# Kernel optimization log

Measured on AMD Instinct MI355X. Metric: run time of the kernel, lower is better.

## Reference

```python
import jax, jax.numpy as jnp
import numpy as np

B, T, DM, DS = 8, 2048, 1024, 256
BASE_DECAY = 0.05


def _lin(k, out_dim, in_dim):
    return jax.random.normal(k, (out_dim, in_dim), jnp.float32) / np.sqrt(in_dim).astype(np.float32)


def setup_inputs() -> dict:
    key = jax.random.key(0)
    ks = jax.random.split(key, 18)
    return {
        "x": jax.random.normal(ks[0], (B, T, DM), jnp.float32),
        "prev_state": jax.random.normal(ks[1], (B, DS), jnp.float32),
        "W_in": _lin(ks[2], DS, DM),
        "W_x": _lin(ks[3], DS, DM),
        "W_s": _lin(ks[4], DS, DS),
        "W_out": _lin(ks[5], DM, DS),
        "W_gx": _lin(ks[6], DS, DM),
        "b_gx": jax.random.normal(ks[7], (DS,), jnp.float32) * 0.02,
        "W_gs": _lin(ks[8], DS, DS),
        "b_gs": jax.random.normal(ks[9], (DS,), jnp.float32) * 0.02,
        "W_dc": _lin(ks[10], DS, DM + DS),
        "b_dc": jax.random.normal(ks[11], (DS,), jnp.float32) * 0.02,
        "W_pp": _lin(ks[12], DS, 2 * DS),
        "b_pp": jax.random.normal(ks[13], (DS,), jnp.float32) * 0.02,
        "W_pg": _lin(ks[14], DS, DS),
        "b_pg": jax.random.normal(ks[15], (DS,), jnp.float32) * 0.02,
    }


def reference(x, prev_state, W_in, W_x, W_s, W_out, W_gx, b_gx, W_gs, b_gs,
              W_dc, b_dc, W_pp, b_pp, W_pg, b_pg):
    # torch Linear: y = x @ W.T (+ b); W is [out, in]
    lin = lambda v, W: jnp.einsum('bti,oi->bto', v, W)
    Bx, Tx, _ = x.shape
    delta = lin(x, W_in)                                   # [B,T,DS]
    s_prev = jnp.broadcast_to(prev_state[:, None, :], (Bx, Tx, prev_state.shape[-1]))
    ctx = jnp.concatenate([x, s_prev], axis=-1)            # [B,T,DM+DS]
    decay = jnp.exp(-BASE_DECAY * jnp.clip(jax.nn.sigmoid(lin(ctx, W_dc) + b_dc), 0.0, 1.0))
    s_pred = s_prev * decay + delta + lin(x, W_x) + 0.5 * lin(s_prev, W_s)
    perturb_in = jnp.concatenate([s_pred, s_prev], axis=-1)  # [B,T,2*DS]
    perturb_vec = jnp.tanh(lin(perturb_in, W_pp) + b_pp)
    perturb_strength = jax.nn.sigmoid(lin(s_prev, W_pg) + b_pg)
    s_corrected = s_pred + perturb_strength * perturb_vec
    gate_in = jax.nn.sigmoid(lin(x, W_gx) + b_gx)
    gate_state = jax.nn.sigmoid(lin(s_prev, W_gs) + b_gs)
    h = s_corrected * gate_in * gate_state
    out = lin(h, W_out)                                    # [B,T,DM]
    return out, h[:, -1, :]
```

## Files before the change

kernel.cpp:

```cpp
#include <hip/hip_runtime.h>
#include <hip/hip_bf16.h>
#include <math.h>


typedef __attribute__((ext_vector_type(4)))  float f32x4;
typedef __attribute__((ext_vector_type(8)))  short bf16x8;

#define DEV static __device__ __forceinline__

DEV float bf2f(short u) {
  union { float f; unsigned i; } v; v.i = ((unsigned)(unsigned short)u) << 16; return v.f;
}
DEV short f2bf(float f) {
  union { float f; unsigned i; } v; v.f = f;
  unsigned x = v.i;
  return (short)((x + 0x7fffu + ((x >> 16) & 1u)) >> 16);
}
DEV unsigned pk_bf16(float lo, float hi) {
  __hip_bfloat162 h = __float22bfloat162_rn(make_float2(lo, hi));
  return *(unsigned*)&h;
}
DEV float sigmoidf_(float x) { return 1.f / (1.f + expf(-x)); }

DEV void gl16(const void* g, void* l) {
  __builtin_amdgcn_global_load_lds(
      (const __attribute__((address_space(1))) void*)(g),
      (__attribute__((address_space(3))) void*)(l), 16, 0, 0);
}

static const size_t OFF_S    = 0;
static const size_t OFF_G    = 8388608;
static const size_t OFF_H    = 16777216;
static const size_t OFF_WCAT = 25165824;
static const size_t OFF_WPP  = OFF_WCAT + 1572864;
static const size_t OFF_WOUT = OFF_WPP + 131072;
static const size_t OFF_VEC  = OFF_WOUT + 524288;

__global__ __launch_bounds__(256, 1) void prep_ws_k(
    const float* __restrict__ W_in, const float* __restrict__ W_x,
    const float* __restrict__ W_gx, const float* __restrict__ W_dc,
    const float* __restrict__ W_pp, const float* __restrict__ W_out,
    short* __restrict__ wcat, short* __restrict__ wpp, short* __restrict__ wout,
    const float* __restrict__ prev, const float* __restrict__ Ws,
    const float* __restrict__ bdc, const float* __restrict__ bpp,
    const float* __restrict__ Wpg, const float* __restrict__ bpg,
    const float* __restrict__ Wgs, const float* __restrict__ bgs,
    float* __restrict__ vecs) {
  const int bid = (int)blockIdx.x, tid = (int)threadIdx.x;
  if (bid < 4352) {
    const int idx = bid * 256 + tid;
    const int N_WCAT = 768 * 1024, N_WPP = 256 * 256;
    if (idx < N_WCAT) {
      const int r = idx >> 10, k = idx & 1023;
      const int g = r / 192, j = r % 192;
      float v;
      if (j < 64)       v = W_in[(g * 64 + j) * 1024 + k] + W_x[(g * 64 + j) * 1024 + k];
      else if (j < 128) v = W_gx[(g * 64 + j - 64) * 1024 + k];
      else              v = W_dc[(g * 64 + j - 128) * 1280 + k];
      wcat[idx] = f2bf(v);
    } else if (idx < N_WCAT + N_WPP) {
      const int j = idx - N_WCAT, o = j >> 8, k = j & 255;
      wpp[j] = f2bf(W_pp[o * 512 + k]);
    } else {
      const int j = idx - N_WCAT - N_WPP, o = j >> 8, k = j & 255;
      wout[j] = f2bf(W_out[o * 256 + k]);
    }
  } else {
    const int sb = bid - 4352;
    const int b = sb / 20, rem = sb % 20, m = rem >> 2, oq = rem & 3;
    const int lane = tid & 63, w = tid >> 6;
    const float4 sv = *(const float4*)(prev + b * 256 + lane * 4);
    const float* Wb; const float* bias; int stride, off;
    if (m == 0)      { Wb = W_dc; stride = 1280; off = 1024; bias = bdc; }
    else if (m == 1) { Wb = Ws;   stride = 256;  off = 0;    bias = nullptr; }
    else if (m == 2) { Wb = W_pp; stride = 512;  off = 256;  bias = bpp; }
    else if (m == 3) { Wb = Wpg;  stride = 256;  off = 0;    bias = bpg; }
    else             { Wb = Wgs;  stride = 256;  off = 0;    bias = bgs; }
    const int o0 = oq * 64 + w * 16;
#pragma unroll 4
    for (int i = 0; i < 16; ++i) {
      const int o = o0 + i;
      const float4 wv = *(const float4*)(Wb + (size_t)o * stride + off + lane * 4);
      float p = wv.x * sv.x + wv.y * sv.y + wv.z * sv.z + wv.w * sv.w;
#pragma unroll
      for (int d = 32; d >= 1; d >>= 1) p += __shfl_xor(p, d, 64);
      if (lane == 0) {
        float r = (m == 1) ? 0.5f * p : p + bias[o];
        if (m >= 3) r = sigmoidf_(r);
        vecs[m * 2048 + b * 256 + o] = r;
      }
    }
  }
}

__global__ __launch_bounds__(512) void gemm1sg_k(const float* __restrict__ X,
                                                 const short* __restrict__ Bm,
                                                 const float* __restrict__ prev,
                                                 const float* __restrict__ bgx,
                                                 const float* __restrict__ vecs,
                                                 short* __restrict__ S,
                                                 short* __restrict__ G) {
  __shared__ short As[2][8192];
  __shared__ short Bs[2][12288];
  const int tid = (int)threadIdx.x, lane = tid & 63, w = tid >> 6;
  int bid = (int)blockIdx.x;
  bid = (bid & 7) * 64 + (bid >> 3);
  const int mt = bid >> 2, grp = bid & 3;
  const int m0 = mt * 128, b = m0 >> 11;
  const short* gB = Bm + (size_t)(grp * 192) * 1024;

  const int GrA[2] = {tid, 512 + tid};
  const int rA0 = GrA[0] >> 3, gA0 = (GrA[0] & 7) ^ (rA0 & 7);
  const int rA1 = GrA[1] >> 3, gA1 = (GrA[1] & 7) ^ (rA1 & 7);
  const float* xr0 = X + (size_t)(m0 + rA0) * 1024 + gA0 * 8;
  const float* xr1 = X + (size_t)(m0 + rA1) * 1024 + gA1 * 8;

  f32x4 acc[12];
#pragma unroll
  for (int ni = 0; ni < 12; ++ni)
#pragma unroll
    for (int r = 0; r < 4; ++r) acc[ni][r] = 0.f;

#define LOADA(va, t)                                                          \
  {                                                                           \
    va[0][0] = *(const float4*)(xr0 + (t) * 64);                              \
    va[0][1] = *(const float4*)(xr0 + (t) * 64 + 4);                          \
    va[1][0] = *(const float4*)(xr1 + (t) * 64);                              \
    va[1][1] = *(const float4*)(xr1 + (t) * 64 + 4);                          \
  }
#define WRITEA(va, buf)                                                       \
  {                                                                           \
    _Pragma("unroll")                                                         \
    for (int j = 0; j < 2; ++j) {                                             \
      uint4 pk;                                                               \
      pk.x = pk_bf16(va[j][0].x, va[j][0].y);                                 \
      pk.y = pk_bf16(va[j][0].z, va[j][0].w);                                 \
      pk.z = pk_bf16(va[j][1].x, va[j][1].y);                                 \
      pk.w = pk_bf16(va[j][1].z, va[j][1].w);                                 \
      *(uint4*)(As[buf] + GrA[j] * 8) = pk;                                   \
    }                                                                         \
  }
#define STGB(buf, t)                                                          \
  {                                                                           \
    _Pragma("unroll")                                                         \
    for (int j = 0; j < 3; ++j) {                                             \
      const int Gr = j * 512 + tid, r = Gr >> 3, g = Gr & 7;                  \
      gl16(gB + (size_t)r * 1024 + (t) * 64 + ((g ^ (r & 7)) * 8),            \
           Bs[buf] + Gr * 8);                                                 \
    }                                                                         \
  }

  {
    float4 va[2][2];
    LOADA(va, 0);
    STGB(0, 0);
    WRITEA(va, 0);
  }
  asm volatile("s_waitcnt vmcnt(0) lgkmcnt(0)" ::: "memory");
  __builtin_amdgcn_s_barrier();

  const int arow = lane & 15, ag = lane >> 4;
  const int rowA = w * 16 + arow;
  const int swzA = rowA & 7;
#pragma unroll 1
  for (int t = 0; t < 16; ++t) {
    const short* sA = As[t & 1];
    const short* sB = Bs[t & 1];
    float4 va[2][2];
    if (t < 15) { LOADA(va, t + 1); STGB((t + 1) & 1, t + 1); }
    bf16x8 af[2];
#pragma unroll
    for (int ks = 0; ks < 2; ++ks)
      af[ks] = *(const bf16x8*)(sA + rowA * 64 + (((ks * 4 + ag) ^ swzA) << 3));
    __builtin_amdgcn_s_setprio(1);
#pragma unroll
    for (int q = 0; q < 3; ++q) {
#pragma unroll
      for (int fj = 0; fj < 4; ++fj) {
        const int r = q * 64 + fj * 16 + arow;
#pragma unroll
        for (int ks = 0; ks < 2; ++ks) {
          const bf16x8 bf = *(const bf16x8*)(sB + r * 64 + (((ks * 4 + ag) ^ (r & 7)) << 3));
          acc[q * 4 + fj] = __builtin_amdgcn_mfma_f32_16x16x32_bf16(
              af[ks], bf, acc[q * 4 + fj], 0, 0, 0);
        }
      }
    }
    __builtin_amdgcn_s_setprio(0);
    if (t < 15) {
      WRITEA(va, (t + 1) & 1);
      asm volatile("s_waitcnt vmcnt(0) lgkmcnt(0)" ::: "memory");
    }
    __builtin_amdgcn_s_barrier();
  }
#undef LOADA
#undef WRITEA
#undef STGB

  const int quad = lane >> 4;
#pragma unroll
  for (int cidx = 0; cidx < 4; ++cidx) {
    const int cg = grp * 64 + cidx * 16 + arow;
    const float sdc = vecs[0 * 2048 + b * 256 + cg];
    const float sws = vecs[1 * 2048 + b * 256 + cg];
    const float pv  = prev[b * 256 + cg];
    const float bg  = bgx[cg];
#pragma unroll
    for (int r = 0; r < 4; ++r) {
      const int row = m0 + w * 16 + quad * 4 + r;
      const float dec = expf(-0.05f * sigmoidf_(acc[8 + cidx][r] + sdc));
      const float sp = pv * dec + acc[cidx][r] + sws;
      const float g = sigmoidf_(acc[4 + cidx][r] + bg);
      S[(size_t)row * 256 + cg] = f2bf(sp);
      G[(size_t)row * 256 + cg] = f2bf(g);
    }
  }
}

__global__ __launch_bounds__(256) void gemm2h_k(const short* __restrict__ S,
                                                const short* __restrict__ G,
                                                const short* __restrict__ Wpp,
                                                const float* __restrict__ vecs,
                                                short* __restrict__ H,
                                                float* __restrict__ out) {
  __shared__ short As2[2][2048];
  __shared__ short Bs2[2][4096];
  const int tid = (int)threadIdx.x, lane = tid & 63, w = tid >> 6;
  const int wr = w >> 1, wc = w & 1;
  int bid = (int)blockIdx.x;
  bid = (bid & 7) * 64 + (bid >> 3);
  const int m0 = (bid >> 1) * 64, n0 = (bid & 1) * 128;
  const int b = m0 >> 11;
  const short* gA = S + (size_t)m0 * 256;
  const short* gB = Wpp + (size_t)n0 * 256;

  f32x4 acc[2][4];
#pragma unroll
  for (int mi = 0; mi < 2; ++mi)
#pragma unroll
    for (int ni = 0; ni < 4; ++ni)
#pragma unroll
      for (int r = 0; r < 4; ++r) acc[mi][ni][r] = 0.f;

#define STAGE2(buf, t)                                                        \
  {                                                                           \
    {                                                                         \
      const int g = tid;                                                      \
      gl16(gA + (size_t)(g >> 2) * 256 + (t) * 32 + (g & 3) * 8,              \
           As2[buf] + w * 512);                                               \
    }                                                                         \
    _Pragma("unroll")                                                         \
    for (int j = 0; j < 2; ++j) {                                             \
      const int g = j * 256 + tid;                                            \
      gl16(gB + (size_t)(g >> 2) * 256 + (t) * 32 + (g & 3) * 8,              \
           Bs2[buf] + (j * 256 + w * 64) * 8);                                \
    }                                                                         \
  }

  STAGE2(0, 0);
  __syncthreads();
  const int arow = lane & 15, ag = lane >> 4;
#pragma unroll 1
  for (int t = 0; t < 8; ++t) {
    if (t < 7) STAGE2((t + 1) & 1, t + 1);
    const short* Asb = As2[t & 1];
    const short* Bsb = Bs2[t & 1];
    bf16x8 af[2], bfv[4];
#pragma unroll
    for (int mi = 0; mi < 2; ++mi)
      af[mi] = *(const bf16x8*)(Asb + (wr * 32 + mi * 16 + arow) * 32 + ag * 8);
#pragma unroll
    for (int ni = 0; ni < 4; ++ni)
      bfv[ni] = *(const bf16x8*)(Bsb + (wc * 64 + ni * 16 + arow) * 32 + ag * 8);
#pragma unroll
    for (int mi = 0; mi < 2; ++mi)
#pragma unroll
      for (int ni = 0; ni < 4; ++ni)
        acc[mi][ni] = __builtin_amdgcn_mfma_f32_16x16x32_bf16(af[mi], bfv[ni], acc[mi][ni], 0, 0, 0);
    __syncthreads();
  }
#undef STAGE2

#pragma unroll
  for (int mi = 0; mi < 2; ++mi)
#pragma unroll
    for (int ni = 0; ni < 4; ++ni) {
      const int col = n0 + wc * 64 + ni * 16 + (lane & 15);
      const float spp  = vecs[2 * 2048 + b * 256 + col];
      const float pstr = vecs[3 * 2048 + b * 256 + col];
      const float gst  = vecs[4 * 2048 + b * 256 + col];
#pragma unroll
      for (int r = 0; r < 4; ++r) {
        const int row = m0 + wr * 32 + mi * 16 + (lane >> 4) * 4 + r;
        const float pv = tanhf(acc[mi][ni][r] + spp);
        const float sp = bf2f(S[(size_t)row * 256 + col]);
        const float h = (sp + pstr * pv) * bf2f(G[(size_t)row * 256 + col]) * gst;
        H[(size_t)row * 256 + col] = f2bf(h);
        if ((row & 2047) == 2047) out[16777216 + b * 256 + col] = h;
      }
    }
}

__global__ __launch_bounds__(256) void gemm3_k(const short* __restrict__ H,
                                               const short* __restrict__ Wout,
                                               float* __restrict__ out) {
  __shared__ short As3[2][2048];
  __shared__ short Bs3[2][8192];
  const int tid = (int)threadIdx.x, lane = tid & 63, w = tid >> 6;
  const int wr = w >> 1, wc = w & 1;
  int bid = (int)blockIdx.x;
  bid = (bid & 7) * 128 + (bid >> 3);
  const int m0 = (bid >> 2) * 64, n0 = (bid & 3) * 256;
  const short* gA = H + (size_t)m0 * 256;
  const short* gB = Wout + (size_t)n0 * 256;

  f32x4 acc[2][8];
#pragma unroll
  for (int mi = 0; mi < 2; ++mi)
#pragma unroll
    for (int ni = 0; ni < 8; ++ni)
#pragma unroll
      for (int r = 0; r < 4; ++r) acc[mi][ni][r] = 0.f;

#define STAGE3(buf, t)                                                        \
  {                                                                           \
    {                                                                         \
      const int g = tid;                                                      \
      gl16(gA + (size_t)(g >> 2) * 256 + (t) * 32 + (g & 3) * 8,              \
           As3[buf] + w * 512);                                               \
    }                                                                         \
    _Pragma("unroll")                                                         \
    for (int j = 0; j < 4; ++j) {                                             \
      const int g = j * 256 + tid;                                            \
      gl16(gB + (size_t)(g >> 2) * 256 + (t) * 32 + (g & 3) * 8,              \
           Bs3[buf] + (j * 256 + w * 64) * 8);                                \
    }                                                                         \
  }

  STAGE3(0, 0);
  __syncthreads();
  const int arow = lane & 15, ag = lane >> 4;
#pragma unroll 1
  for (int t = 0; t < 8; ++t) {
    if (t < 7) STAGE3((t + 1) & 1, t + 1);
    const short* Asb = As3[t & 1];
    const short* Bsb = Bs3[t & 1];
    bf16x8 af[2], bfv[8];
#pragma unroll
    for (int mi = 0; mi < 2; ++mi)
      af[mi] = *(const bf16x8*)(Asb + (wr * 32 + mi * 16 + arow) * 32 + ag * 8);
#pragma unroll
    for (int ni = 0; ni < 8; ++ni)
      bfv[ni] = *(const bf16x8*)(Bsb + (wc * 128 + ni * 16 + arow) * 32 + ag * 8);
#pragma unroll
    for (int mi = 0; mi < 2; ++mi)
#pragma unroll
      for (int ni = 0; ni < 8; ++ni)
        acc[mi][ni] = __builtin_amdgcn_mfma_f32_16x16x32_bf16(af[mi], bfv[ni], acc[mi][ni], 0, 0, 0);
    __syncthreads();
  }
#undef STAGE3

#pragma unroll
  for (int mi = 0; mi < 2; ++mi)
#pragma unroll
    for (int ni = 0; ni < 8; ++ni) {
      const int col = n0 + wc * 128 + ni * 16 + (lane & 15);
#pragma unroll
      for (int r = 0; r < 4; ++r) {
        const int row = m0 + wr * 32 + mi * 16 + (lane >> 4) * 4 + r;
        out[(size_t)row * 1024 + col] = acc[mi][ni][r];
      }
    }
}

extern "C" void kernel_launch(void* const* d_in, const int* in_sizes, int n_in,
                              void* d_out, int out_size, void* d_ws, size_t ws_size,
                              hipStream_t stream) {
  (void)in_sizes; (void)n_in; (void)out_size; (void)ws_size;
  const float* x      = (const float*)d_in[0];
  const float* prev   = (const float*)d_in[1];
  const float* W_in   = (const float*)d_in[2];
  const float* W_x    = (const float*)d_in[3];
  const float* W_s    = (const float*)d_in[4];
  const float* W_out  = (const float*)d_in[5];
  const float* W_gx   = (const float*)d_in[6];
  const float* b_gx   = (const float*)d_in[7];
  const float* W_gs   = (const float*)d_in[8];
  const float* b_gs   = (const float*)d_in[9];
  const float* W_dc   = (const float*)d_in[10];
  const float* b_dc   = (const float*)d_in[11];
  const float* W_pp   = (const float*)d_in[12];
  const float* b_pp   = (const float*)d_in[13];
  const float* W_pg   = (const float*)d_in[14];
  const float* b_pg   = (const float*)d_in[15];

  char* ws = (char*)d_ws;
  short* S    = (short*)(ws + OFF_S);
  short* G    = (short*)(ws + OFF_G);
  short* H    = (short*)(ws + OFF_H);
  short* wcat = (short*)(ws + OFF_WCAT);
  short* wpp  = (short*)(ws + OFF_WPP);
  short* wout = (short*)(ws + OFF_WOUT);
  float* vecs = (float*)(ws + OFF_VEC);
  float* out  = (float*)d_out;

  prep_ws_k<<<4512, 256, 0, stream>>>(W_in, W_x, W_gx, W_dc, W_pp, W_out,
                                      wcat, wpp, wout, prev, W_s, b_dc, b_pp,
                                      W_pg, b_pg, W_gs, b_gs, vecs);
  gemm1sg_k<<<512, 512, 0, stream>>>(x, wcat, prev, b_gx, vecs, S, G);
  gemm2h_k<<<512, 256, 0, stream>>>(S, G, wpp, vecs, H, out);
  gemm3_k<<<1024, 256, 0, stream>>>(H, wout, out);
}
```

Measured before the change: 97.38 us.

## Prefetch X tile two stages ahead in registers with partial vmcnt waits

Restructures the first GEMM's main loop so the fp32 X tile is loaded into registers two K-steps ahead, with two register sets alternating across a manually unrolled pair of iterations. The per-iteration wait drops from vmcnt(0) to vmcnt(4), so the newest X loads can stay in flight across the barrier while the B tile and the previous X tile are consumed. The goal is to hide global-load latency of the activation stream. In exchange it raises register pressure and relies on exact vmcnt accounting; a wrong count would cause silent races.

After: 105.5 us. 8.4% more time.

```diff
diff --git a/kernel.cpp b/kernel.cpp
--- a/kernel.cpp
+++ b/kernel.cpp
@@ -109,9 +109,9 @@
   const int m0 = mt * 128, b = m0 >> 11;
   const short* gB = Bm + (size_t)(grp * 192) * 1024;
 
-  const int GrA[2] = {tid, 512 + tid};
-  const int rA0 = GrA[0] >> 3, gA0 = (GrA[0] & 7) ^ (rA0 & 7);
-  const int rA1 = GrA[1] >> 3, gA1 = (GrA[1] & 7) ^ (rA1 & 7);
+  const int Gr0 = tid, Gr1 = 512 + tid;
+  const int rA0 = Gr0 >> 3, gA0 = (Gr0 & 7) ^ (rA0 & 7);
+  const int rA1 = Gr1 >> 3, gA1 = (Gr1 & 7) ^ (rA1 & 7);
   const float* xr0 = X + (size_t)(m0 + rA0) * 1024 + gA0 * 8;
   const float* xr1 = X + (size_t)(m0 + rA1) * 1024 + gA1 * 8;
 
@@ -130,15 +130,17 @@
   }
 #define WRITEA(va, buf)                                                       \
   {                                                                           \
-    _Pragma("unroll")                                                         \
-    for (int j = 0; j < 2; ++j) {                                             \
-      uint4 pk;                                                               \
-      pk.x = pk_bf16(va[j][0].x, va[j][0].y);                                 \
-      pk.y = pk_bf16(va[j][0].z, va[j][0].w);                                 \
-      pk.z = pk_bf16(va[j][1].x, va[j][1].y);                                 \
-      pk.w = pk_bf16(va[j][1].z, va[j][1].w);                                 \
-      *(uint4*)(As[buf] + GrA[j] * 8) = pk;                                   \
-    }                                                                         \
+    uint4 pk0, pk1;                                                           \
+    pk0.x = pk_bf16(va[0][0].x, va[0][0].y);                                  \
+    pk0.y = pk_bf16(va[0][0].z, va[0][0].w);                                  \
+    pk0.z = pk_bf16(va[0][1].x, va[0][1].y);                                  \
+    pk0.w = pk_bf16(va[0][1].z, va[0][1].w);                                  \
+    pk1.x = pk_bf16(va[1][0].x, va[1][0].y);                                  \
+    pk1.y = pk_bf16(va[1][0].z, va[1][0].w);                                  \
+    pk1.z = pk_bf16(va[1][1].x, va[1][1].y);                                  \
+    pk1.w = pk_bf16(va[1][1].z, va[1][1].w);                                  \
+    *(uint4*)(As[buf] + Gr0 * 8) = pk0;                                       \
+    *(uint4*)(As[buf] + Gr1 * 8) = pk1;                                       \
   }
 #define STGB(buf, t)                                                          \
   {                                                                           \
@@ -150,49 +152,64 @@
     }                                                                         \
   }
 
+  float4 va[2][2], vb[2][2];
   {
-    float4 va[2][2];
-    LOADA(va, 0);
+    float4 v0[2][2];
+    LOADA(v0, 0);
     STGB(0, 0);
-    WRITEA(va, 0);
-  }
-  asm volatile("s_waitcnt vmcnt(0) lgkmcnt(0)" ::: "memory");
+    WRITEA(v0, 0);
+    LOADA(va, 1);
+  }
+  asm volatile("s_waitcnt vmcnt(4) lgkmcnt(0)" ::: "memory");
   __builtin_amdgcn_s_barrier();
 
   const int arow = lane & 15, ag = lane >> 4;
   const int rowA = w * 16 + arow;
   const int swzA = rowA & 7;
+
+#define TILE_BODY(t, sAb, sBb, dAb, dBb, vcur, vnext)                         \
+  {                                                                           \
+    const short* sA = As[sAb];                                                \
+    const short* sB = Bs[sBb];                                                \
+    if ((t) < 15) STGB(dBb, (t) + 1);                                         \
+    __builtin_amdgcn_sched_barrier(0);       \
+    if ((t) + 2 < 16) LOADA(vnext, (t) + 2);                                  \
+    bf16x8 af[2];                                                             \
+    _Pragma("unroll")                                                         \
+    for (int ks = 0; ks < 2; ++ks)                                            \
+      af[ks] = *(const bf16x8*)(sA + rowA * 64 + (((ks * 4 + ag) ^ swzA) << 3)); \
+    __builtin_amdgcn_s_setprio(1);                                            \
+    _Pragma("unroll")                                                         \
+    for (int q = 0; q < 3; ++q) {                                             \
+      _Pragma("unroll")                                                       \
+      for (int fj = 0; fj < 4; ++fj) {                                        \
+        const int r = q * 64 + fj * 16 + arow;                                \
+        _Pragma("unroll")                                                     \
+        for (int ks = 0; ks < 2; ++ks) {                                      \
+          const bf16x8 bf = *(const bf16x8*)(sB + r * 64 +                    \
+                                             (((ks * 4 + ag) ^ (r & 7)) << 3)); \
+          acc[q * 4 + fj] = __builtin_amdgcn_mfma_f32_16x16x32_bf16(          \
+              af[ks], bf, acc[q * 4 + fj], 0, 0, 0);                          \
+        }                                                                     \
+      }                                                                       \
+    }                                                                         \
+    __builtin_amdgcn_s_setprio(0);                                            \
+    if ((t) < 15) WRITEA(vcur, dAb);         \
+    if ((t) < 14) {                                                           \
+      asm volatile("s_waitcnt vmcnt(4) lgkmcnt(0)" ::: "memory");             \
+    } else if ((t) == 14) {                                                   \
+      asm volatile("s_waitcnt vmcnt(0) lgkmcnt(0)" ::: "memory");             \
+    }                                                                         \
+    __builtin_amdgcn_s_barrier();                                             \
+  }
+
 #pragma unroll 1
-  for (int t = 0; t < 16; ++t) {
-    const short* sA = As[t & 1];
-    const short* sB = Bs[t & 1];
-    float4 va[2][2];
-    if (t < 15) { LOADA(va, t + 1); STGB((t + 1) & 1, t + 1); }
-    bf16x8 af[2];
-#pragma unroll
-    for (int ks = 0; ks < 2; ++ks)
-      af[ks] = *(const bf16x8*)(sA + rowA * 64 + (((ks * 4 + ag) ^ swzA) << 3));
-    __builtin_amdgcn_s_setprio(1);
-#pragma unroll
-    for (int q = 0; q < 3; ++q) {
-#pragma unroll
-      for (int fj = 0; fj < 4; ++fj) {
-        const int r = q * 64 + fj * 16 + arow;
-#pragma unroll
-        for (int ks = 0; ks < 2; ++ks) {
-          const bf16x8 bf = *(const bf16x8*)(sB + r * 64 + (((ks * 4 + ag) ^ (r & 7)) << 3));
-          acc[q * 4 + fj] = __builtin_amdgcn_mfma_f32_16x16x32_bf16(
-              af[ks], bf, acc[q * 4 + fj], 0, 0, 0);
-        }
-      }
-    }
-    __builtin_amdgcn_s_setprio(0);
-    if (t < 15) {
-      WRITEA(va, (t + 1) & 1);
-      asm volatile("s_waitcnt vmcnt(0) lgkmcnt(0)" ::: "memory");
-    }
-    __builtin_amdgcn_s_barrier();
-  }
+  for (int tt = 0; tt < 8; ++tt) {
+    const int t0 = 2 * tt, t1 = 2 * tt + 1;
+    TILE_BODY(t0, 0, 0, 1, 1, va, vb);
+    TILE_BODY(t1, 1, 1, 0, 0, vb, va);
+  }
+#undef TILE_BODY
 #undef LOADA
 #undef WRITEA
 #undef STGB
```
